# Performance work log

Hardware: AMD Instinct MI355X
Metric: run time of the kernel (lower is better)

Reference implementation:

```python
import jax, jax.numpy as jnp
import numpy as np

F_THRESHOLD = 10  # zero out DCT coefficients with i + j <= 10 (low-frequency triangle)


def _dct_mat(N):
    # torch_dct.dct with norm=None: X_k = 2 * sum_n x_n cos(pi*(2n+1)*k/(2N))
    n = np.arange(N)
    k = np.arange(N)[:, None]
    return (2.0 * np.cos(np.pi * (2 * n + 1) * k / (2 * N))).astype(np.float32)  # [k, n]


def _idct_mat(N):
    # inverse of the norm=None DCT-II above: x_n = (1/N) * sum_k w_k X_k cos(pi*(2n+1)*k/(2N)), w_0=0.5
    n = np.arange(N)[:, None]
    k = np.arange(N)
    w = np.ones(N, dtype=np.float64)
    w[0] = 0.5
    return ((w * np.cos(np.pi * (2 * n + 1) * k / (2 * N))) / N).astype(np.float32)  # [n, k]


def _filtermask(H, W):
    i = jnp.arange(H)[:, None]
    j = jnp.arange(W)[None, :]
    return jnp.where(i + j <= F_THRESHOLD, 0.0, 1.0).astype(jnp.float32)  # [H, W]


def setup_inputs() -> dict:
    key = jax.random.key(0)
    im = jax.random.normal(key, (32, 3, 512, 512), dtype=jnp.float32)
    return {"im": im}


def reference(im) -> jnp.ndarray:
    B, C, H, W = im.shape
    Ch = jnp.asarray(_dct_mat(H))   # [kh, h]
    Cw = jnp.asarray(_dct_mat(W))   # [kw, w]
    Dh = jnp.asarray(_idct_mat(H))  # [h, kh]
    Dw = jnp.asarray(_idct_mat(W))  # [w, kw]
    mask = _filtermask(H, W)

    # dct_2d: DCT-II along W then along H
    x = jnp.einsum('kh,bchw,lw->bckl', Ch, im, Cw)
    x = x * mask  # zero low-frequency triangle
    # idct_2d
    x = jnp.einsum('hk,bckl,wl->bchw', Dh, x, Dw)
    return x
```

## Files before the change

kernel.cpp:

```cpp
#include <hip/hip_runtime.h>
#include <math.h>

#define NPIX 512
#define NK 11
#define NPAIR 121
#define RBLKS 8
#define NCH 96

#define PI_F 3.14159265358979323846f

__device__ inline void build_Cs(float (*Cs)[NPIX], int t) {
#pragma unroll
    for (int i = t; i < NK * NPIX; i += 256) {
        int k = i >> 9;
        int h = i & 511;
        int m = ((2 * h + 1) * k) & 2047;
        float ang = (float)m * (PI_F / 1024.0f);
        ((float*)Cs)[i] = 2.0f * cosf(ang);
    }
}

#define AS_LD 516
__global__ __launch_bounds__(256) void k_partial(const float* __restrict__ im,
                                                 float* __restrict__ plow) {
    __shared__ float Cs[NK][NPIX];
    __shared__ float As[NK][AS_LD];

    int bid = blockIdx.x;
    int c = bid >> 3, rb = bid & 7;
    int t = threadIdx.x;

    build_Cs(Cs, t);
    __syncthreads();

    int half = t >> 7;
    int col4 = t & 127;
    int w0 = col4 * 4;
    int rowbase = rb * 64 + half * 32;
    const float* imc = im + (size_t)c * NPIX * NPIX;

    float a[NK][4];
#pragma unroll
    for (int k = 0; k < NK; ++k)
        for (int j = 0; j < 4; ++j) a[k][j] = 0.f;

    for (int i = 0; i < 32; ++i) {
        int h = rowbase + i;
        float4 v = *(const float4*)(imc + (size_t)h * NPIX + w0);
#pragma unroll
        for (int k = 0; k < NK; ++k) {
            float ch = Cs[k][h];
            a[k][0] += ch * v.x;
            a[k][1] += ch * v.y;
            a[k][2] += ch * v.z;
            a[k][3] += ch * v.w;
        }
    }

    if (half == 0) {
#pragma unroll
        for (int k = 0; k < NK; ++k)
            *(float4*)&As[k][w0] = make_float4(a[k][0], a[k][1], a[k][2], a[k][3]);
    }
    __syncthreads();
    if (half == 1) {
#pragma unroll
        for (int k = 0; k < NK; ++k) {
            float4 cur = *(float4*)&As[k][w0];
            cur.x += a[k][0]; cur.y += a[k][1]; cur.z += a[k][2]; cur.w += a[k][3];
            *(float4*)&As[k][w0] = cur;
        }
    }
    __syncthreads();

    int k = t >> 4;
    int sub = t & 15;
    if (k < NK) {
        float* outp = plow + (size_t)bid * NPAIR + k * NK;
        for (int l = 0; l < NK; ++l) {
            float acc = 0.f;
#pragma unroll
            for (int wi = 0; wi < 32; ++wi) {
                int w = wi * 16 + sub;
                acc += As[k][w] * Cs[l][w];
            }
            acc += __shfl_xor(acc, 8);
            acc += __shfl_xor(acc, 4);
            acc += __shfl_xor(acc, 2);
            acc += __shfl_xor(acc, 1);
            if (sub == 0) outp[l] = acc;
        }
    }
}

__global__ __launch_bounds__(256) void k_output(const float* __restrict__ im,
                                                const float* __restrict__ plow,
                                                float* __restrict__ out) {
    __shared__ float Cs[NK][NPIX];
    __shared__ float Ls[NPAIR];

    int bid = blockIdx.x;
    int c = bid >> 3, rb = bid & 7;
    int t = threadIdx.x;

    build_Cs(Cs, t);

    if (t < NPAIR) {
        int k = t / NK, l = t % NK;
        float s = 0.f;
        const float* pp = plow + (size_t)c * RBLKS * NPAIR + t;
#pragma unroll
        for (int b = 0; b < RBLKS; ++b) s += pp[b * NPAIR];
        float sk = (k == 0 ? 0.5f : 1.0f) * (1.0f / 1024.0f);
        float sl = (l == 0 ? 0.5f : 1.0f) * (1.0f / 1024.0f);
        Ls[t] = (k + l <= 10) ? s * sk * sl : 0.f;
    }
    __syncthreads();

    int half = t >> 7;
    int col4 = t & 127;
    int w0 = col4 * 4;
    int rowbase = rb * 64 + half * 32;

    float B[NK][4];
#pragma unroll
    for (int k = 0; k < NK; ++k)
        for (int j = 0; j < 4; ++j) B[k][j] = 0.f;

#pragma unroll
    for (int l = 0; l < NK; ++l) {
        float4 cl = *(const float4*)&Cs[l][w0];
#pragma unroll
        for (int k = 0; k < NK; ++k) {
            float lw = Ls[k * NK + l];
            B[k][0] += lw * cl.x;
            B[k][1] += lw * cl.y;
            B[k][2] += lw * cl.z;
            B[k][3] += lw * cl.w;
        }
    }

    const float* imc = im + (size_t)c * NPIX * NPIX;
    float* outc = out + (size_t)c * NPIX * NPIX;

    for (int i = 0; i < 32; ++i) {
        int h = rowbase + i;
        float4 v = *(const float4*)(imc + (size_t)h * NPIX + w0);
        float c0 = 0.f, c1 = 0.f, c2 = 0.f, c3 = 0.f;
#pragma unroll
        for (int k = 0; k < NK; ++k) {
            float ch = Cs[k][h];
            c0 += ch * B[k][0];
            c1 += ch * B[k][1];
            c2 += ch * B[k][2];
            c3 += ch * B[k][3];
        }
        float4 o = make_float4(v.x - c0, v.y - c1, v.z - c2, v.w - c3);
        *(float4*)(outc + (size_t)h * NPIX + w0) = o;
    }
}

extern "C" void kernel_launch(void* const* d_in, const int* in_sizes, int n_in,
                              void* d_out, int out_size, void* d_ws, size_t ws_size,
                              hipStream_t stream) {
    const float* im = (const float*)d_in[0];
    float* out = (float*)d_out;
    float* plow = (float*)d_ws;

    k_partial<<<NCH * RBLKS, 256, 0, stream>>>(im, plow);
    k_output<<<NCH * RBLKS, 256, 0, stream>>>(im, plow, out);
}
```

Before: 67.35 us.

## Transpose cosine table, use hardware cos, and shuffle-reduce partial DCT

Stores the cosine table transposed as [h][12], so each row's eleven coefficients come in as three float4 LDS reads instead of eleven scalar reads. The table is built with the native AMD revolution-based cos builtin instead of cosf. In the partial kernel, the shared As staging plus second-pass dot products is replaced by computing the w-direction DCT in registers with on-the-fly cosines, followed by a wave-shuffle and LDS reduction. The output kernel also skips terms outside the low-frequency triangle and unrolls the row loops. The hardware cos may be slightly less accurate, and the register-side l loop adds many shuffles.

```diff
diff --git a/kernel.cpp b/kernel.cpp
--- a/kernel.cpp
+++ b/kernel.cpp
@@ -3,107 +3,111 @@
 
 #define NPIX 512
 #define NK 11
+#define NKP 12
 #define NPAIR 121
 #define RBLKS 8
 #define NCH 96
 
-#define PI_F 3.14159265358979323846f
+#if __has_builtin(__builtin_amdgcn_cosf)
+__device__ inline float cos_rev(float rev) { return __builtin_amdgcn_cosf(rev); }
+#else
+__device__ inline float cos_rev(float rev) { return __cosf(rev * 6.28318530717958647692f); }
+#endif
 
-__device__ inline void build_Cs(float (*Cs)[NPIX], int t) {
+__device__ inline float ctab(int h, int k) {
+    int m = ((2 * h + 1) * k) & 2047;
+    return 2.0f * cos_rev((float)m * (1.0f / 2048.0f));
+}
+
+__device__ inline void build_Cst(float (*Cst)[NKP], int t) {
+    float* f = (float*)Cst;
 #pragma unroll
-    for (int i = t; i < NK * NPIX; i += 256) {
-        int k = i >> 9;
-        int h = i & 511;
-        int m = ((2 * h + 1) * k) & 2047;
-        float ang = (float)m * (PI_F / 1024.0f);
-        ((float*)Cs)[i] = 2.0f * cosf(ang);
+    for (int i = t; i < NPIX * NKP; i += 256) {
+        int h = i / NKP;
+        int k = i - h * NKP;
+        f[i] = (k < NK) ? ctab(h, k) : 0.f;
     }
 }
 
-#define AS_LD 516
 __global__ __launch_bounds__(256) void k_partial(const float* __restrict__ im,
                                                  float* __restrict__ plow) {
-    __shared__ float Cs[NK][NPIX];
-    __shared__ float As[NK][AS_LD];
+    __shared__ float Cst[NPIX][NKP];
+    __shared__ float red[16][NPAIR];
 
     int bid = blockIdx.x;
     int c = bid >> 3, rb = bid & 7;
     int t = threadIdx.x;
 
-    build_Cs(Cs, t);
+    build_Cst(Cst, t);
     __syncthreads();
 
     int half = t >> 7;
     int col4 = t & 127;
     int w0 = col4 * 4;
     int rowbase = rb * 64 + half * 32;
-    const float* imc = im + (size_t)c * NPIX * NPIX;
+    const float* imc = im + (size_t)c * NPIX * NPIX + (size_t)rowbase * NPIX + w0;
 
     float a[NK][4];
 #pragma unroll
     for (int k = 0; k < NK; ++k)
         for (int j = 0; j < 4; ++j) a[k][j] = 0.f;
 
+#pragma unroll 4
     for (int i = 0; i < 32; ++i) {
         int h = rowbase + i;
-        float4 v = *(const float4*)(imc + (size_t)h * NPIX + w0);
+        float4 v = *(const float4*)(imc + (size_t)i * NPIX);
+        const float4* crow = (const float4*)&Cst[h][0];
+        float4 c0 = crow[0], c1 = crow[1], c2 = crow[2];
+        float ck[12];
+        *(float4*)&ck[0] = c0; *(float4*)&ck[4] = c1; *(float4*)&ck[8] = c2;
 #pragma unroll
         for (int k = 0; k < NK; ++k) {
-            float ch = Cs[k][h];
-            a[k][0] += ch * v.x;
-            a[k][1] += ch * v.y;
-            a[k][2] += ch * v.z;
-            a[k][3] += ch * v.w;
+            a[k][0] += ck[k] * v.x;
+            a[k][1] += ck[k] * v.y;
+            a[k][2] += ck[k] * v.z;
+            a[k][3] += ck[k] * v.w;
         }
     }
 
-    if (half == 0) {
+#pragma unroll
+    for (int l = 0; l < NK; ++l) {
+        float cl0 = ctab(w0 + 0, l);
+        float cl1 = ctab(w0 + 1, l);
+        float cl2 = ctab(w0 + 2, l);
+        float cl3 = ctab(w0 + 3, l);
+        float pk[NK];
 #pragma unroll
         for (int k = 0; k < NK; ++k)
-            *(float4*)&As[k][w0] = make_float4(a[k][0], a[k][1], a[k][2], a[k][3]);
-    }
-    __syncthreads();
-    if (half == 1) {
+            pk[k] = a[k][0] * cl0 + a[k][1] * cl1 + a[k][2] * cl2 + a[k][3] * cl3;
 #pragma unroll
-        for (int k = 0; k < NK; ++k) {
-            float4 cur = *(float4*)&As[k][w0];
-            cur.x += a[k][0]; cur.y += a[k][1]; cur.z += a[k][2]; cur.w += a[k][3];
-            *(float4*)&As[k][w0] = cur;
-        }
+        for (int s = 1; s <= 8; s <<= 1)
+#pragma unroll
+            for (int k = 0; k < NK; ++k) pk[k] += __shfl_xor(pk[k], s);
+        if ((t & 15) == 0)
+#pragma unroll
+            for (int k = 0; k < NK; ++k) red[t >> 4][k * NK + l] = pk[k];
     }
     __syncthreads();
 
-    int k = t >> 4;
-    int sub = t & 15;
-    if (k < NK) {
-        float* outp = plow + (size_t)bid * NPAIR + k * NK;
-        for (int l = 0; l < NK; ++l) {
-            float acc = 0.f;
+    if (t < NPAIR) {
+        float s = 0.f;
 #pragma unroll
-            for (int wi = 0; wi < 32; ++wi) {
-                int w = wi * 16 + sub;
-                acc += As[k][w] * Cs[l][w];
-            }
-            acc += __shfl_xor(acc, 8);
-            acc += __shfl_xor(acc, 4);
-            acc += __shfl_xor(acc, 2);
-            acc += __shfl_xor(acc, 1);
-            if (sub == 0) outp[l] = acc;
-        }
+        for (int g = 0; g < 16; ++g) s += red[g][t];
+        plow[(size_t)bid * NPAIR + t] = s;
     }
 }
 
 __global__ __launch_bounds__(256) void k_output(const float* __restrict__ im,
                                                 const float* __restrict__ plow,
                                                 float* __restrict__ out) {
-    __shared__ float Cs[NK][NPIX];
+    __shared__ float Cst[NPIX][NKP];
     __shared__ float Ls[NPAIR];
 
     int bid = blockIdx.x;
     int c = bid >> 3, rb = bid & 7;
     int t = threadIdx.x;
 
-    build_Cs(Cs, t);
+    build_Cst(Cst, t);
 
     if (t < NPAIR) {
         int k = t / NK, l = t % NK;
@@ -129,34 +133,42 @@
 
 #pragma unroll
     for (int l = 0; l < NK; ++l) {
-        float4 cl = *(const float4*)&Cs[l][w0];
+        float cl0 = ctab(w0 + 0, l);
+        float cl1 = ctab(w0 + 1, l);
+        float cl2 = ctab(w0 + 2, l);
+        float cl3 = ctab(w0 + 3, l);
 #pragma unroll
         for (int k = 0; k < NK; ++k) {
+            if (k + l > 10) break;
             float lw = Ls[k * NK + l];
-            B[k][0] += lw * cl.x;
-            B[k][1] += lw * cl.y;
-            B[k][2] += lw * cl.z;
-            B[k][3] += lw * cl.w;
+            B[k][0] += lw * cl0;
+            B[k][1] += lw * cl1;
+            B[k][2] += lw * cl2;
+            B[k][3] += lw * cl3;
         }
     }
 
-    const float* imc = im + (size_t)c * NPIX * NPIX;
-    float* outc = out + (size_t)c * NPIX * NPIX;
+    const float* imc = im + (size_t)c * NPIX * NPIX + (size_t)rowbase * NPIX + w0;
+    float* outc = out + (size_t)c * NPIX * NPIX + (size_t)rowbase * NPIX + w0;
 
+#pragma unroll 4
     for (int i = 0; i < 32; ++i) {
         int h = rowbase + i;
-        float4 v = *(const float4*)(imc + (size_t)h * NPIX + w0);
-        float c0 = 0.f, c1 = 0.f, c2 = 0.f, c3 = 0.f;
+        float4 v = *(const float4*)(imc + (size_t)i * NPIX);
+        const float4* crow = (const float4*)&Cst[h][0];
+        float4 c0 = crow[0], c1 = crow[1], c2 = crow[2];
+        float ck[12];
+        *(float4*)&ck[0] = c0; *(float4*)&ck[4] = c1; *(float4*)&ck[8] = c2;
+        float r0 = 0.f, r1 = 0.f, r2 = 0.f, r3 = 0.f;
 #pragma unroll
         for (int k = 0; k < NK; ++k) {
-            float ch = Cs[k][h];
-            c0 += ch * B[k][0];
-            c1 += ch * B[k][1];
-            c2 += ch * B[k][2];
-            c3 += ch * B[k][3];
+            r0 += ck[k] * B[k][0];
+            r1 += ck[k] * B[k][1];
+            r2 += ck[k] * B[k][2];
+            r3 += ck[k] * B[k][3];
         }
-        float4 o = make_float4(v.x - c0, v.y - c1, v.z - c2, v.w - c3);
-        *(float4*)(outc + (size_t)h * NPIX + w0) = o;
+        float4 o = make_float4(v.x - r0, v.y - r1, v.z - r2, v.w - r3);
+        *(float4*)(outc + (size_t)i * NPIX) = o;
     }
 }
 
```

After: 72.21 us. +7.2%, slower.
